# Kernel tuning notes

Hardware: AMD Instinct MI355X
Metric: run time of the kernel (lower is better)

Reference implementation:

```python
import jax, jax.numpy as jnp
import numpy as np

N_NODES = 100000
N_EDGES = 600000
C = 16          # n_in_channels
H = 3 * C       # edge hidden width
NOUT = 1        # n_out_channels
L = 5           # n_hidden_layer


def _mlp(x, w0, b0, wh, bh):
    # input layer + L hidden layers, ReLU activations
    h = jax.nn.relu(x @ w0 + b0)
    for l in range(wh.shape[0]):
        h = jax.nn.relu(h @ wh[l] + bh[l])
    return h


def _node_conv(x, src, dst, angles, w0, b0, wh, bh, n_nodes):
    # gather endpoint features + per-edge angle, MLP, mean-scatter to target nodes
    msg = _mlp(jnp.concatenate([x[dst], x[src], angles], axis=-1), w0, b0, wh, bh)
    agg = jax.ops.segment_sum(msg, dst, num_segments=n_nodes)
    cnt = jax.ops.segment_sum(jnp.ones((src.shape[0], 1), x.dtype), dst, num_segments=n_nodes)
    return agg / jnp.maximum(cnt, 1.0)


def _edge_conv(x, src, dst, e_init, w0, b0, wh, bh, wc, bc):
    # symmetric per-edge embedding from both endpoint orders; side loss enforces symmetry
    f1 = _mlp(jnp.concatenate([x[dst], x[src]], axis=-1), w0, b0, wh, bh)
    f2 = _mlp(jnp.concatenate([x[src], x[dst]], axis=-1), w0, b0, wh, bh)
    side_loss = jnp.mean((f1 - f2) ** 2)
    fe = 0.5 * (f1 + f2)
    out = jnp.concatenate([fe, e_init], axis=-1) @ wc + bc
    return side_loss, out


def setup_inputs() -> dict:
    key = jax.random.key(0)
    ks = jax.random.split(key, 32)

    def w(k, shape):
        fan_in = shape[-2] if len(shape) > 1 else shape[-1]
        return (jax.random.normal(k, shape, jnp.float32) / np.sqrt(fan_in)).astype(jnp.float32)

    d = {}
    d['node_features'] = jax.random.normal(ks[0], (N_NODES, C), jnp.float32)
    d['edge_index'] = jax.random.randint(ks[1], (2, N_EDGES), 0, N_NODES)
    d['angles'] = jax.random.normal(ks[2], (N_EDGES, 1), jnp.float32)
    d['gt_edges'] = jax.random.uniform(ks[3], (N_EDGES,), jnp.float32)
    d['actions'] = jax.random.normal(ks[4], (N_EDGES, 1), jnp.float32)
    i = 5
    for k in (1, 2):  # NodeConv1 / NodeConv2: in 2C+1 (x_i,x_j,angle) -> C, L hidden CxC
        d[f'nc{k}_w0'] = w(ks[i], (2 * C + 1, C)); d[f'nc{k}_b0'] = jnp.zeros((C,), jnp.float32)
        d[f'nc{k}_wh'] = w(ks[i + 1], (L, C, C)); d[f'nc{k}_bh'] = jnp.zeros((L, C), jnp.float32)
        i += 2
    # EdgeConv1: node-pair MLP 2C->H, combine with 1-ch actions -> H (3*n_in)
    # EdgeConv2: node-pair MLP 2C->H, combine with H-ch init edge feats -> NOUT
    for k, (cin, ccomb, cout) in {1: (2 * C, H + 1, H), 2: (2 * C, 2 * H, NOUT)}.items():
        d[f'ec{k}_w0'] = w(ks[i], (cin, H)); d[f'ec{k}_b0'] = jnp.zeros((H,), jnp.float32)
        d[f'ec{k}_wh'] = w(ks[i + 1], (L, H, H)); d[f'ec{k}_bh'] = jnp.zeros((L, H), jnp.float32)
        d[f'ec{k}_wc'] = w(ks[i + 2], (ccomb, cout)); d[f'ec{k}_bc'] = jnp.zeros((cout,), jnp.float32)
        i += 3
    return d


def reference(node_features, edge_index, angles, gt_edges, actions,
              nc1_w0, nc1_b0, nc1_wh, nc1_bh,
              nc2_w0, nc2_b0, nc2_wh, nc2_bh,
              ec1_w0, ec1_b0, ec1_wh, ec1_bh, ec1_wc, ec1_bc,
              ec2_w0, ec2_b0, ec2_wh, ec2_bh, ec2_wc, ec2_bc):
    src, dst = edge_index[0], edge_index[1]
    n_nodes = node_features.shape[0]
    x = _node_conv(node_features, src, dst, angles, nc1_w0, nc1_b0, nc1_wh, nc1_bh, n_nodes)
    sl1, ef = _edge_conv(x, src, dst, actions, ec1_w0, ec1_b0, ec1_wh, ec1_bh, ec1_wc, ec1_bc)
    x = _node_conv(x, src, dst, angles, nc2_w0, nc2_b0, nc2_wh, nc2_bh, n_nodes)
    sl2, ef = _edge_conv(x, src, dst, ef, ec2_w0, ec2_b0, ec2_wh, ec2_bh, ec2_wc, ec2_bc)
    side_loss = (sl1 + sl2) / 2
    return ef, side_loss
```

## Files before the change

kernel.cpp:

```cpp
#include <hip/hip_runtime.h>

typedef unsigned int u32;
typedef _Float16 f16;
typedef __attribute__((ext_vector_type(8))) _Float16 f16x8;
typedef __attribute__((ext_vector_type(4))) _Float16 f16x4;
typedef __attribute__((ext_vector_type(4))) float f32x4;

#define NNODES 100000
#define NEDGES 600000
#define CC 16
#define HH 48
#define NL 5
#define ECNB 9375
#define NBS 391

#define OX1   0
#define OX2   800000
#define ODSTP 800000
#define OAGG  1600000
#define OSCAN 1600000
#define ORANK 1601024
#define OROW  3200000
#define ODEG  3300032
#define OGF   3300032
#define OPERM 3400032
#define OSL   4000032
#define WS_NEED_FLOATS 4000064

__global__ __launch_bounds__(256) void count_deg(const int* __restrict__ ei,
    int* __restrict__ deg, int* __restrict__ rank){
  int e = blockIdx.x * 256 + threadIdx.x;
  if (e >= NEDGES) return;
  rank[e] = atomicAdd(&deg[ei[NEDGES + e]], 1);
}

__global__ __launch_bounds__(256) void scan_p1(const int* __restrict__ deg, int* __restrict__ bsum){
  __shared__ int red[256];
  int b = blockIdx.x, t = threadIdx.x;
  int i = b * 256 + t;
  red[t] = (i < NNODES) ? deg[i] : 0;
  __syncthreads();
  for (int off = 128; off; off >>= 1){
    if (t < off) red[t] += red[t + off];
    __syncthreads();
  }
  if (t == 0) bsum[b] = red[0];
}

__global__ __launch_bounds__(512) void scan_p2(const int* __restrict__ bsum,
    int* __restrict__ boff, int* __restrict__ rowptr){
  __shared__ int s[512];
  int t = threadIdx.x;
  s[t] = (t < NBS) ? bsum[t] : 0;
  __syncthreads();
  for (int off = 1; off < 512; off <<= 1){
    int v = (t >= off) ? s[t - off] : 0;
    __syncthreads();
    s[t] += v;
    __syncthreads();
  }
  if (t < NBS) boff[t] = (t == 0) ? 0 : s[t - 1];
  if (t == 0) rowptr[NNODES] = s[NBS - 1];
}

__global__ __launch_bounds__(256) void scan_p3(const int* __restrict__ deg,
    const int* __restrict__ boff, int* __restrict__ rowptr){
  __shared__ int s[256];
  int b = blockIdx.x, t = threadIdx.x;
  int i = b * 256 + t;
  int d = (i < NNODES) ? deg[i] : 0;
  s[t] = d;
  __syncthreads();
  for (int off = 1; off < 256; off <<= 1){
    int v = (t >= off) ? s[t - off] : 0;
    __syncthreads();
    s[t] += v;
    __syncthreads();
  }
  if (i < NNODES) rowptr[i] = boff[b] + s[t] - d;
}

__global__ __launch_bounds__(256) void scatter_perm(const int* __restrict__ ei,
    const int* __restrict__ rowptr, const int* __restrict__ rank,
    int* __restrict__ perm, int* __restrict__ dstp){
  int e = blockIdx.x * 256 + threadIdx.x;
  if (e >= NEDGES) return;
  int d = ei[NEDGES + e];
  int pos = rowptr[d] + rank[e];
  perm[pos] = e;
  dstp[pos] = d;
}

__global__ void fin_loss(const float* __restrict__ slacc, float* __restrict__ out){
  out[NEDGES] = slacc[0] * (1.0f / 57600000.0f);
}

__global__ __launch_bounds__(256) void prep_wfrag(
    const float* __restrict__ e1w0, const float* __restrict__ e1wh, const float* __restrict__ e1wc,
    const float* __restrict__ e2w0, const float* __restrict__ e2wh, f16* __restrict__ gf)
{
  int idx = blockIdx.x * 256 + threadIdx.x;
  if (idx >= 39936) return;
  int j = idx & 7, lane = (idx >> 3) & 63, f = idx >> 9;
  int wt = f % 3, ksl = f / 3;
  int ks = ksl & 1, lay = ksl >> 1;
  int k = ks * 32 + ((lane >> 4) << 3) + j;
  int m = wt * 16 + (lane & 15);
  const float* w; int Kl;
  if (lay == 0){ w = e1w0; Kl = 32; }
  else if (lay <= 5){ w = e1wh + (lay - 1) * 2304; Kl = 48; }
  else if (lay == 6){ w = e1wc; Kl = 48; }
  else if (lay == 7){ w = e2w0; Kl = 32; }
  else { w = e2wh + (lay - 8) * 2304; Kl = 48; }
  gf[idx] = (k < Kl) ? (f16)w[k * 48 + m] : (f16)0.f;
}

__global__ __launch_bounds__(256) void prep_wfrag_nc(
    const float* __restrict__ n1w0, const float* __restrict__ n1wh,
    const float* __restrict__ n2w0, const float* __restrict__ n2wh,
    f16* __restrict__ gfn)
{
  int idx = blockIdx.x * 256 + threadIdx.x;
  if (idx >= 24 * 512) return;
  int j = idx & 7, lane = (idx >> 3) & 63, f = idx >> 9;
  int conv = f / 12, slot = f % 12;
  int kq = ((lane >> 4) << 3) + j;
  int m = lane & 15;
  const float* w0 = conv ? n2w0 : n1w0;
  const float* wh = conv ? n2wh : n1wh;
  float val;
  bool wantLo;
  if (slot <= 1){
    val = w0[kq * 16 + m];
    wantLo = (slot == 1);
  } else {
    int l = (slot - 2) >> 1;
    bool isB = (slot - 2) & 1;
    const float* wl = wh + l * 256;
    if (!isB){ val = wl[(kq & 15) * 16 + m]; wantLo = false; }
    else if (kq < 16){ val = wl[kq * 16 + m]; wantLo = true; }
    else { gfn[idx] = (f16)0.f; return; }
  }
  f16 hi = (f16)val;
  gfn[idx] = wantLo ? (f16)(val - (float)hi) : hi;
}

template<bool FP32IN>
__global__ __launch_bounds__(256, 4) void nc_mfma(
    const void* __restrict__ xin, const int* __restrict__ ei,
    const float* __restrict__ ang, const int* __restrict__ perm,
    const int* __restrict__ dstp,
    const f16* __restrict__ gfn,
    const float* __restrict__ w0f,
    const float* __restrict__ b0, const float* __restrict__ bh,
    float* __restrict__ agg)
{
  constexpr int RW  = FP32IN ? 64 : 32;
  constexpr int RSH = FP32IN ? 6  : 5;
  constexpr int RSM = FP32IN ? 7  : 3;
  __shared__ __align__(16) f16 Hn[256 * RW];

  const int t = threadIdx.x, lane = t & 63, wv = t >> 6;
  const int q = lane >> 4, n15 = lane & 15;
  const int base = blockIdx.x * 256;

  int pev[4]; int dkv[4]; float angv[4];
  #pragma unroll
  for (int et = 0; et < 4; et++){
    int gi = base + wv * 64 + et * 16 + n15;
    int gic = gi < NEDGES ? gi : NEDGES - 1;
    pev[et] = perm[gic];
    dkv[et] = dstp[gic];
  }

  {
    int peO = (q == 0) ? pev[0] : (q == 1) ? pev[1] : (q == 2) ? pev[2] : pev[3];
    int dO  = (q == 0) ? dkv[0] : (q == 1) ? dkv[1] : (q == 2) ? dkv[2] : dkv[3];
    int rs = t & RSM;
    f16* hp = &Hn[t << RSH];
    if (FP32IN){
      const float* xf = (const float*)xin;
      const float4* pd = (const float4*)(xf + (long)dO * 16);
      int sO = ei[peO];
      const float4* ps = (const float4*)(xf + (long)sO * 16);
      #pragma unroll
      for (int c = 0; c < 4; c++){
        const float4* pp = (c < 2) ? pd : ps;
        float4 va = pp[(c & 1) * 2];
        float4 vb = pp[(c & 1) * 2 + 1];
        float xv8[8] = {va.x, va.y, va.z, va.w, vb.x, vb.y, vb.z, vb.w};
        f16x8 hi8, lo8;
        #pragma unroll
        for (int k = 0; k < 8; k++){
          float v = xv8[k];
          f16 h = (f16)v;
          hi8[k] = h;
          lo8[k] = (f16)(v - (float)h);
        }
        *(f16x8*)&hp[(c ^ rs) << 3]       = hi8;
        *(f16x8*)&hp[((c + 4) ^ rs) << 3] = lo8;
      }
    } else {
      const f16* xh = (const f16*)xin;
      f16x8 r0 = *(const f16x8*)&xh[(long)dO * 16];
      f16x8 r1 = *(const f16x8*)&xh[(long)dO * 16 + 8];
      int sO = ei[peO];
      f16x8 r2 = *(const f16x8*)&xh[(long)sO * 16];
      f16x8 r3 = *(const f16x8*)&xh[(long)sO * 16 + 8];
      *(f16x8*)&hp[(0 ^ rs) << 3] = r0;
      *(f16x8*)&hp[(1 ^ rs) << 3] = r1;
      *(f16x8*)&hp[(2 ^ rs) << 3] = r2;
      *(f16x8*)&hp[(3 ^ rs) << 3] = r3;
    }
  }
  #pragma unroll
  for (int et = 0; et < 4; et++) angv[et] = ang[pev[et]];

  float4 wang = *(const float4*)&w0f[32 * 16 + 4 * q];

  f32x4 C[4];
  for (int lay = 0; lay < 6; lay++){
    const float* bp = (lay == 0) ? b0 : &bh[(lay - 1) * 16];
    float4 b4 = *(const float4*)&bp[4 * q];
    #pragma unroll
    for (int et = 0; et < 4; et++){
      C[et] = (f32x4){b4.x, b4.y, b4.z, b4.w};
      if (lay == 0){
        float a = angv[et];
        C[et][0] += a * wang.x; C[et][1] += a * wang.y;
        C[et][2] += a * wang.z; C[et][3] += a * wang.w;
      }
    }
    const int nst = (lay == 0) ? (FP32IN ? 3 : 2) : 2;
    #pragma unroll 3
    for (int st = 0; st < nst; st++){
      int fr, cb;
      if (lay == 0){
        if (FP32IN){ fr = (st == 2) ? 1 : 0; cb = (st == 1) ? 4 : 0; }
        else       { fr = st; cb = 0; }
      }
      else { fr = 2 + 2 * (lay - 1) + st; cb = 0; }
      f16x8 Af = *(const f16x8*)&gfn[(fr << 9) + (lane << 3)];
      int c = cb + q;
      #pragma unroll
      for (int et = 0; et < 4; et++){
        int r = wv * 64 + et * 16 + n15;
        f16x8 Bf = *(const f16x8*)&Hn[(r << RSH) + ((c ^ (r & RSM)) << 3)];
        C[et] = __builtin_amdgcn_mfma_f32_16x16x32_f16(Af, Bf, C[et], 0, 0, 0);
      }
    }
    if (lay < 5){
      #pragma unroll
      for (int et = 0; et < 4; et++){
        int r = wv * 64 + et * 16 + n15;
        f16x4 hi4, lo4;
        #pragma unroll
        for (int reg = 0; reg < 4; reg++){
          float v = fmaxf(C[et][reg], 0.f);
          f16 h = (f16)v;
          hi4[reg] = h;
          lo4[reg] = (f16)(v - (float)h);
        }
        int ch = 4 * q;
        *(f16x4*)&Hn[(r << RSH) + ((((ch >> 3) ^ (r & RSM)) << 3) | (ch & 7))] = hi4;
        int cl = 16 + 4 * q;
        *(f16x4*)&Hn[(r << RSH) + ((((cl >> 3) ^ (r & RSM)) << 3) | (cl & 7))] = lo4;
      }
    } else {
      #pragma unroll
      for (int et = 0; et < 4; et++){
        int li = wv * 64 + et * 16 + n15;
        bool valid = (base + li) < NEDGES;
        int dk = valid ? dkv[et] : -1;
        bool sm[4];
        int o = 1;
        #pragma unroll
        for (int k2 = 0; k2 < 4; k2++, o <<= 1){
          int dn = __shfl_down(dk, o);
          sm[k2] = (n15 + o < 16) && (dn == dk);
        }
        int dprev = __shfl_up(dk, 1);
        bool head = valid && ((n15 == 0) || (dprev != dk));
        #pragma unroll
        for (int reg = 0; reg < 4; reg++){
          float v = valid ? fmaxf(C[et][reg], 0.f) : 0.f;
          o = 1;
          #pragma unroll
          for (int k2 = 0; k2 < 4; k2++, o <<= 1){
            float vn = __shfl_down(v, o);
            if (sm[k2]) v += vn;
          }
          if (head) atomicAdd(&agg[(long)dk * 16 + 4 * q + reg], v);
        }
      }
    }
  }
}

__global__ __launch_bounds__(256) void node_finh(
    float* __restrict__ agg, const int* __restrict__ rowptr, f16* __restrict__ xh)
{
  int n = blockIdx.x * 256 + threadIdx.x;
  if (n >= NNODES) return;
  float inv = 1.f / fmaxf((float)(rowptr[n+1] - rowptr[n]), 1.f);
  float4* ap = (float4*)&agg[(long)n * 16];
  float4 z = {0.f, 0.f, 0.f, 0.f};
  f16x8 o0, o1;
  #pragma unroll
  for (int k = 0; k < 2; k++){
    float4 v = ap[k];
    o0[4*k] = (f16)(v.x*inv); o0[4*k+1] = (f16)(v.y*inv);
    o0[4*k+2] = (f16)(v.z*inv); o0[4*k+3] = (f16)(v.w*inv);
    ap[k] = z;
  }
  #pragma unroll
  for (int k = 0; k < 2; k++){
    float4 v = ap[2+k];
    o1[4*k] = (f16)(v.x*inv); o1[4*k+1] = (f16)(v.y*inv);
    o1[4*k+2] = (f16)(v.z*inv); o1[4*k+3] = (f16)(v.w*inv);
    ap[2+k] = z;
  }
  *(f16x8*)&xh[(long)n * 16]     = o0;
  *(f16x8*)&xh[(long)n * 16 + 8] = o1;
}

__global__ __launch_bounds__(256, 5) void ec_mfma(
    const f16* __restrict__ xh1, const f16* __restrict__ xh2,
    const int* __restrict__ ei,
    const float* __restrict__ act, const f16* __restrict__ gf,
    const float* __restrict__ e1wc, const float* __restrict__ e1b0,
    const float* __restrict__ e1bh, const float* __restrict__ e1bc,
    const float* __restrict__ e2b0, const float* __restrict__ e2bh,
    const float* __restrict__ e2wc, const float* __restrict__ e2bc,
    float* __restrict__ outG, float* __restrict__ slacc)
{
  __shared__ __align__(16) f16 Hb[128 * 64];
  __shared__ float sred[4];

  const int t = threadIdx.x;
  const int lane = t & 63;
  const int wv = t >> 6;
  const int q = lane >> 4, n15 = lane & 15;
  const int eidx = (lane >> 1) & 15;
  const int fh   = lane >> 5;
  const int sub  = lane & 1;
  const int myrow = fh * 64 + wv * 16 + eidx;
  const int gebase = blockIdx.x * 64;

  const int node = ei[((fh ^ sub) ? 0 : NEDGES) + gebase + wv * 16 + eidx];
  const int e2 = gebase + wv * 16 + n15;
  const float aL = act[e2];

  const int rs = myrow & 7;
  auto store_lds = [&](const f16* __restrict__ xh){
    f16x8 pa0 = *(const f16x8*)&xh[(long)node * 16];
    f16x8 pa1 = *(const f16x8*)&xh[(long)node * 16 + 8];
    f16* hp = &Hb[myrow << 6];
    *(f16x8*)&hp[((2*sub)     ^ rs) << 3] = pa0;
    *(f16x8*)&hp[((2*sub + 1) ^ rs) << 3] = pa1;
    if (sub){
      f16x8 z = {};
      *(f16x8*)&hp[(6 ^ rs) << 3] = z;
      *(f16x8*)&hp[(7 ^ rs) << 3] = z;
    }
  };

  float side = 0.f;
  float outAcc = 0.f;

  auto layer = [&](int lay, const float* bias, int nks, int mode){
    const int nEt = (mode == 2) ? 1 : 2;
    f32x4 C[3][2];
    #pragma unroll
    for (int wt = 0; wt < 3; wt++){
      float4 b4 = *(const float4*)&bias[wt*16 + 4*q];
      C[wt][0] = (f32x4){b4.x, b4.y, b4.z, b4.w};
      C[wt][1] = C[wt][0];
    }
    for (int ks = 0; ks < nks; ks++){
      int c = ks*4 + q;
      f16x8 Af[3];
      #pragma unroll
      for (int wt = 0; wt < 3; wt++)
        Af[wt] = *(const f16x8*)&gf[((((lay*2 + ks)*3) + wt) << 9) + (lane << 3)];
      for (int et = 0; et < nEt; et++){
        int r = (et << 6) + wv*16 + n15;
        f16x8 Bf = *(const f16x8*)&Hb[(r << 6) + ((c ^ (r & 7)) << 3)];
        #pragma unroll
        for (int wt = 0; wt < 3; wt++)
          C[wt][et] = __builtin_amdgcn_mfma_f32_16x16x32_f16(Af[wt], Bf, C[wt][et], 0, 0, 0);
      }
    }
    if (mode == 0){
      #pragma unroll
      for (int et = 0; et < 2; et++){
        int r = (et << 6) + wv*16 + n15;
        #pragma unroll
        for (int wt = 0; wt < 3; wt++){
          f16x4 pk;
          #pragma unroll
          for (int reg = 0; reg < 4; reg++) pk[reg] = (f16)fmaxf(C[wt][et][reg], 0.f);
          int col = wt*16 + 4*q;
          *(f16x4*)&Hb[(r << 6) + ((((col >> 3) ^ (r & 7)) << 3) | (col & 7))] = pk;
        }
      }
    } else if (mode == 1){
      int r = wv*16 + n15;
      #pragma unroll
      for (int wt = 0; wt < 3; wt++){
        f16x4 pk;
        #pragma unroll
        for (int reg = 0; reg < 4; reg++){
          float v1 = fmaxf(C[wt][0][reg], 0.f);
          float v2 = fmaxf(C[wt][1][reg], 0.f);
          float dd = v1 - v2; side += dd * dd;
          pk[reg] = (f16)(0.5f * (v1 + v2));
        }
        int col = wt*16 + 4*q;
        *(f16x4*)&Hb[(r << 6) + ((((col >> 3) ^ (r & 7)) << 3) | (col & 7))] = pk;
      }
    } else if (mode == 2){
      #pragma unroll
      for (int wt = 0; wt < 3; wt++){
        float4 wr = *(const float4*)&e1wc[2304 + wt*16 + 4*q];
        float4 wb = *(const float4*)&e2wc[48 + wt*16 + 4*q];
        outAcc += (C[wt][0][0] + aL * wr.x) * wb.x
                + (C[wt][0][1] + aL * wr.y) * wb.y
                + (C[wt][0][2] + aL * wr.z) * wb.z
                + (C[wt][0][3] + aL * wr.w) * wb.w;
      }
    } else {
      #pragma unroll
      for (int wt = 0; wt < 3; wt++){
        float4 wa = *(const float4*)&e2wc[wt*16 + 4*q];
        float av[4] = {wa.x, wa.y, wa.z, wa.w};
        #pragma unroll
        for (int reg = 0; reg < 4; reg++){
          float v1 = fmaxf(C[wt][0][reg], 0.f);
          float v2 = fmaxf(C[wt][1][reg], 0.f);
          float dd = v1 - v2; side += dd * dd;
          float fe = 0.5f * (v1 + v2);
          outAcc += fe * av[reg];
        }
      }
    }
  };

  store_lds(xh1);

  layer(0, e1b0,        1, 0);
  layer(1, e1bh + 0*48, 2, 0);
  layer(2, e1bh + 1*48, 2, 0);
  layer(3, e1bh + 2*48, 2, 0);
  layer(4, e1bh + 3*48, 2, 0);
  layer(5, e1bh + 4*48, 2, 1);
  layer(6, e1bc,        2, 2);

  store_lds(xh2);

  layer(7,  e2b0,        1, 0);
  layer(8,  e2bh + 0*48, 2, 0);
  layer(9,  e2bh + 1*48, 2, 0);
  layer(10, e2bh + 2*48, 2, 0);
  layer(11, e2bh + 3*48, 2, 0);
  layer(12, e2bh + 4*48, 2, 3);

  {
    float v = outAcc;
    v += __shfl_xor(v, 16);
    v += __shfl_xor(v, 32);
    if (lane < 16) outG[e2] = v + e2bc[0];
  }

  float sv = side;
  #pragma unroll
  for (int off = 32; off; off >>= 1) sv += __shfl_down(sv, off);
  if (lane == 0) sred[wv] = sv;
  __syncthreads();
  if (t == 0) atomicAdd(slacc, sred[0] + sred[1] + sred[2] + sred[3]);
}

extern "C" void kernel_launch(void* const* d_in, const int* in_sizes, int n_in,
                              void* d_out, int out_size, void* d_ws, size_t ws_size,
                              hipStream_t stream)
{
  if (n_in < 25) return;
  if (ws_size < (size_t)WS_NEED_FLOATS * sizeof(float)) return;

  const float* nf  = (const float*)d_in[0];
  const int*   ei  = (const int*)d_in[1];
  const float* ang = (const float*)d_in[2];
  const float* act = (const float*)d_in[4];
  const float* nc1_w0 = (const float*)d_in[5];
  const float* nc1_b0 = (const float*)d_in[6];
  const float* nc1_wh = (const float*)d_in[7];
  const float* nc1_bh = (const float*)d_in[8];
  const float* nc2_w0 = (const float*)d_in[9];
  const float* nc2_b0 = (const float*)d_in[10];
  const float* nc2_wh = (const float*)d_in[11];
  const float* nc2_bh = (const float*)d_in[12];
  const float* e1w0 = (const float*)d_in[13];
  const float* e1b0 = (const float*)d_in[14];
  const float* e1wh = (const float*)d_in[15];
  const float* e1bh = (const float*)d_in[16];
  const float* e1wc = (const float*)d_in[17];
  const float* e1bc = (const float*)d_in[18];
  const float* e2w0 = (const float*)d_in[19];
  const float* e2b0 = (const float*)d_in[20];
  const float* e2wh = (const float*)d_in[21];
  const float* e2bh = (const float*)d_in[22];
  const float* e2wc = (const float*)d_in[23];
  const float* e2bc = (const float*)d_in[24];

  float* ws  = (float*)d_ws;
  float* out = (float*)d_out;

  f16* xh1    = (f16*)(ws + OX1);
  f16* xh2    = (f16*)(ws + OX2);
  int* dstp   = (int*)(ws + ODSTP);
  float* agg  = ws + OAGG;
  int* rowptr = (int*)(ws + OROW);
  int* deg    = (int*)(ws + ODEG);
  f16* gf     = (f16*)(ws + OGF);
  f16* gfn    = gf + 39936;
  int* bsum   = (int*)(ws + OSCAN);
  int* boff   = bsum + 512;
  int* rank   = (int*)(ws + ORANK);
  int* perm   = (int*)(ws + OPERM);
  float* sl   = ws + OSL;

  const int eb  = (NEDGES + 255) / 256;
  const int nbN = (NNODES + 255) / 256;
  const int pfb = (39936 + 255) / 256;
  const int pnb = (12288 + 255) / 256;

  (void)hipMemsetAsync(deg, 0, (size_t)NNODES * sizeof(int), stream);
  (void)hipMemsetAsync(sl, 0, sizeof(float), stream);

  hipLaunchKernelGGL(count_deg, dim3(eb), dim3(256), 0, stream, ei, deg, rank);
  hipLaunchKernelGGL(scan_p1, dim3(NBS), dim3(256), 0, stream, deg, bsum);
  hipLaunchKernelGGL(scan_p2, dim3(1), dim3(512), 0, stream, bsum, boff, rowptr);
  hipLaunchKernelGGL(scan_p3, dim3(NBS), dim3(256), 0, stream, deg, boff, rowptr);
  hipLaunchKernelGGL(scatter_perm, dim3(eb), dim3(256), 0, stream, ei, rowptr, rank, perm, dstp);

  hipLaunchKernelGGL(prep_wfrag, dim3(pfb), dim3(256), 0, stream,
      e1w0, e1wh, e1wc, e2w0, e2wh, gf);
  hipLaunchKernelGGL(prep_wfrag_nc, dim3(pnb), dim3(256), 0, stream,
      nc1_w0, nc1_wh, nc2_w0, nc2_wh, gfn);

  (void)hipMemsetAsync(agg, 0, (size_t)NNODES * 16 * sizeof(float), stream);
  hipLaunchKernelGGL((nc_mfma<true>), dim3(eb), dim3(256), 0, stream,
      (const void*)nf, ei, ang, perm, dstp, gfn, nc1_w0, nc1_b0, nc1_bh, agg);
  hipLaunchKernelGGL(node_finh, dim3(nbN), dim3(256), 0, stream, agg, rowptr, xh1);

  hipLaunchKernelGGL((nc_mfma<false>), dim3(eb), dim3(256), 0, stream,
      (const void*)xh1, ei, ang, perm, dstp, gfn + 12 * 512, nc2_w0, nc2_b0, nc2_bh, agg);
  hipLaunchKernelGGL(node_finh, dim3(nbN), dim3(256), 0, stream, agg, rowptr, xh2);

  hipLaunchKernelGGL(ec_mfma, dim3(ECNB), dim3(256), 0, stream,
      xh1, xh2, ei, act, gf,
      e1wc, e1b0, e1bh, e1bc, e2b0, e2bh, e2wc, e2bc,
      out, sl);

  hipLaunchKernelGGL(fin_loss, dim3(1), dim3(1), 0, stream, sl, out);
}
```

Baseline: 442.3 us.

## Double-buffer edge-MLP weight fragments through LDS with per-step block barriers

Waves 0-2 of each block now prefetch the next k-step's MFMA weight fragments from global memory into a two-slot LDS buffer, instead of every wave reading them directly from global memory. The aim is to cut redundant global/L2 weight loads and hide their latency behind the current step's MFMAs. In exchange, a __syncthreads is added after every k-step (24 per block), which forces the previously independent waves into lockstep. It also adds 6 KB of LDS per block, which may lower occupancy.

```diff
diff --git a/kernel.cpp b/kernel.cpp
--- a/kernel.cpp
+++ b/kernel.cpp
@@ -335,7 +335,11 @@
     float* __restrict__ outG, float* __restrict__ slacc)
 {
   __shared__ __align__(16) f16 Hb[128 * 64];
+  __shared__ __align__(16) f16 Wb[2][1536];
   __shared__ float sred[4];
+
+  constexpr int KSL[24] = {0, 2,3, 4,5, 6,7, 8,9, 10,11, 12,13, 14,
+                           16,17, 18,19, 20,21, 22,23, 24,25};
 
   const int t = threadIdx.x;
   const int lane = t & 63;
@@ -350,6 +354,15 @@
   const int node = ei[((fh ^ sub) ? 0 : NEDGES) + gebase + wv * 16 + eidx];
   const int e2 = gebase + wv * 16 + n15;
   const float aL = act[e2];
+
+  auto stage = [&](int step){
+    if (step >= 24) return;
+    if (wv < 3){
+      int ksl = KSL[step];
+      f16x8 w = *(const f16x8*)&gf[((ksl * 3 + wv) << 9) + (lane << 3)];
+      *(f16x8*)&Wb[step & 1][(wv << 9) + (lane << 3)] = w;
+    }
+  };
 
   const int rs = myrow & 7;
   auto store_lds = [&](const f16* __restrict__ xh){
@@ -368,7 +381,7 @@
   float side = 0.f;
   float outAcc = 0.f;
 
-  auto layer = [&](int lay, const float* bias, int nks, int mode){
+  auto layer = [&](int lay, int s0, const float* bias, int nks, int mode){
     const int nEt = (mode == 2) ? 1 : 2;
     f32x4 C[3][2];
     #pragma unroll
@@ -378,11 +391,13 @@
       C[wt][1] = C[wt][0];
     }
     for (int ks = 0; ks < nks; ks++){
+      int step = s0 + ks;
+      stage(step + 1);
       int c = ks*4 + q;
       f16x8 Af[3];
       #pragma unroll
       for (int wt = 0; wt < 3; wt++)
-        Af[wt] = *(const f16x8*)&gf[((((lay*2 + ks)*3) + wt) << 9) + (lane << 3)];
+        Af[wt] = *(const f16x8*)&Wb[step & 1][(wt << 9) + (lane << 3)];
       for (int et = 0; et < nEt; et++){
         int r = (et << 6) + wv*16 + n15;
         f16x8 Bf = *(const f16x8*)&Hb[(r << 6) + ((c ^ (r & 7)) << 3)];
@@ -390,6 +405,7 @@
         for (int wt = 0; wt < 3; wt++)
           C[wt][et] = __builtin_amdgcn_mfma_f32_16x16x32_f16(Af[wt], Bf, C[wt][et], 0, 0, 0);
       }
+      __syncthreads();
     }
     if (mode == 0){
       #pragma unroll
@@ -447,23 +463,25 @@
   };
 
   store_lds(xh1);
-
-  layer(0, e1b0,        1, 0);
-  layer(1, e1bh + 0*48, 2, 0);
-  layer(2, e1bh + 1*48, 2, 0);
-  layer(3, e1bh + 2*48, 2, 0);
-  layer(4, e1bh + 3*48, 2, 0);
-  layer(5, e1bh + 4*48, 2, 1);
-  layer(6, e1bc,        2, 2);
+  stage(0);
+  __syncthreads();
+
+  layer(0, 0,  e1b0,        1, 0);
+  layer(1, 1,  e1bh + 0*48, 2, 0);
+  layer(2, 3,  e1bh + 1*48, 2, 0);
+  layer(3, 5,  e1bh + 2*48, 2, 0);
+  layer(4, 7,  e1bh + 3*48, 2, 0);
+  layer(5, 9,  e1bh + 4*48, 2, 1);
+  layer(6, 11, e1bc,        2, 2);
 
   store_lds(xh2);
 
-  layer(7,  e2b0,        1, 0);
-  layer(8,  e2bh + 0*48, 2, 0);
-  layer(9,  e2bh + 1*48, 2, 0);
-  layer(10, e2bh + 2*48, 2, 0);
-  layer(11, e2bh + 3*48, 2, 0);
-  layer(12, e2bh + 4*48, 2, 3);
+  layer(7,  13, e2b0,        1, 0);
+  layer(8,  14, e2bh + 0*48, 2, 0);
+  layer(9,  16, e2bh + 1*48, 2, 0);
+  layer(10, 18, e2bh + 2*48, 2, 0);
+  layer(11, 20, e2bh + 3*48, 2, 0);
+  layer(12, 22, e2bh + 4*48, 2, 3);
 
   {
     float v = outAcc;
```

Result: slower. 470.6 us (+6.4%).
